# Kernel optimization log

Measured on AMD Instinct MI355X. Metric: run time of the kernel, lower is better.

## Reference

```python
import jax, jax.numpy as jnp
import numpy as np

BN_EPS = 1e-5


def setup_inputs() -> dict:
    key = jax.random.key(0)
    k1, k2, k3 = jax.random.split(key, 3)
    B, Fin, N, Fout, k = 8, 64, 4096, 128, 16
    x = jax.random.normal(k1, (B, Fin, N), dtype=jnp.float32)
    # 1x1 conv weight [Fout, 2*Fin] and bias [Fout]
    W = jax.random.normal(k2, (Fout, 2 * Fin), dtype=jnp.float32) * (1.0 / np.sqrt(2 * Fin))
    b = jax.random.normal(k3, (Fout,), dtype=jnp.float32) * 0.01
    gamma = jnp.ones((Fout,), dtype=jnp.float32)
    beta = jnp.zeros((Fout,), dtype=jnp.float32)
    return {"x": x, "W": W, "b": b, "gamma": gamma, "beta": beta, "k": k}


def reference(x, W, b, gamma, beta, k):
    # x: [B, Fin, N]
    B, Fin, N = x.shape
    xt = jnp.transpose(x, (0, 2, 1))  # [B, N, Fin]
    # pairwise squared distances [B, N, N]
    sq = jnp.sum(xt * xt, axis=-1)  # [B, N]
    dist = sq[:, :, None] + sq[:, None, :] - 2.0 * jnp.einsum("bnf,bmf->bnm", xt, xt)
    # k nearest neighbours excluding self (smallest dist is self ~ 0)
    _, idx = jax.lax.top_k(-dist, k + 1)  # [B, N, k+1]
    idx = idx[:, :, 1:]  # [B, N, k]
    # gather neighbour features: [B, N, k, Fin]
    neigh = jax.vmap(lambda pts, ids: pts[ids])(xt, idx)
    central = xt[:, :, None, :]  # [B, N, 1, Fin]
    edge = jnp.concatenate(
        [jnp.broadcast_to(central, neigh.shape), neigh - central], axis=-1
    )  # [B, N, k, 2*Fin]
    # 1x1 conv == channel contraction
    y = jnp.einsum("bnkc,oc->bnko", edge, W) + b  # [B, N, k, Fout]
    # BatchNorm2d (training-mode batch stats over B, N, k per channel)
    mean = jnp.mean(y, axis=(0, 1, 2))
    var = jnp.var(y, axis=(0, 1, 2))
    y = (y - mean) * jax.lax.rsqrt(var + BN_EPS) * gamma + beta
    y = jax.nn.relu(y)
    # max over k neighbours -> [B, Fout, N]
    out = jnp.max(y, axis=2)  # [B, N, Fout]
    return jnp.transpose(out, (0, 2, 1))
```

## Files before the change

kernel.cpp:

```cpp
#include <hip/hip_runtime.h>

#define NPTS 4096
#define FIN  64
#define FOUT 128
#define KNB  16
#define BATCH 8
#define BN_EPS 1e-5f
#define FINF 1e30f

#define OFF_SQ     (0)
#define OFF_IDX    (OFF_SQ + BATCH*NPTS*4)
#define OFF_PART   (OFF_IDX + BATCH*NPTS*KNB*4)
#define OFF_PART2  (OFF_PART + 512*FOUT*4)
#define OFF_UBAR   (OFF_PART2 + 512*FOUT*4)
#define OFF_VT     (OFF_UBAR + BATCH*NPTS*FOUT*4)

__global__ __launch_bounds__(256) void uvsq_kernel(const float* __restrict__ x, const float* __restrict__ W,
                                                   const float* __restrict__ bias,
                                                   float* __restrict__ ubar, float* __restrict__ vt,
                                                   float* __restrict__ sqout){
  const int t = threadIdx.x, l = t & 63;
  const int w = __builtin_amdgcn_readfirstlane(t >> 6);
  const int bid = blockIdx.x;
  const int b = bid & 7, grp = bid >> 3;
  const int n = grp*64 + l;
  const float* xp = x + (size_t)b*FIN*NPTS + n;
  float xc[FIN];
  float s = 0.f;
  #pragma unroll
  for (int f=0; f<FIN; ++f){ xc[f] = xp[(size_t)f*NPTS]; s = fmaf(xc[f], xc[f], s); }
  const size_t bn = (size_t)b*NPTS + n;
  if (w == 0) sqout[bn] = s;
  float* up = ubar + bn*FOUT;
  float* vp = vt   + bn*FOUT;
  for (int o = w*32; o < w*32+32; ++o){
    const float* wr = W + o*2*FIN;
    float a1=0.f, a2=0.f;
    #pragma unroll
    for (int f=0; f<FIN; ++f){ a1 = fmaf(wr[f], xc[f], a1); a2 = fmaf(wr[FIN+f], xc[f], a2); }
    up[o] = a1 - a2 + bias[o];
    vp[o] = a2;
  }
}

__global__ __launch_bounds__(256,2) void knn_kernel(const float* __restrict__ x, const float* __restrict__ sq,
                                                    int* __restrict__ idxout){
  __shared__ float xt[2*64*64];
  __shared__ float rowf[64*68];
  __shared__ float dtile[64*68];
  __shared__ float rowsq[64];
  const int t = threadIdx.x;
  const int w = t >> 6;
  const int l = t & 63;
  const int b  = blockIdx.x & 7;
  const int n0 = (blockIdx.x >> 3) * 64;
  const float* xb  = x  + (size_t)b*FIN*NPTS;
  const float* sqb = sq + b*NPTS;

  for (int j=t; j<4096; j+=256){ int row = j & 63, f = j >> 6; rowf[row*68+f] = xb[(size_t)f*NPTS + n0 + row]; }
  if (t < 64) rowsq[t] = sqb[n0 + t];

  const int c4 = (t & 15) << 2;
  const int tf = t >> 4;

  float4 pre[4];
  #pragma unroll
  for (int it=0; it<4; ++it) pre[it] = *(const float4*)(xb + (size_t)(it*16 + tf)*NPTS + c4);
  #pragma unroll
  for (int it=0; it<4; ++it){
    const int f = it*16 + tf;
    const float4 v = pre[it];
    xt[(c4+0)*64 + (f ^ c4)] = v.x;
    xt[(c4+1)*64 + (f ^ c4)] = v.y;
    xt[(c4+2)*64 + (f ^ c4)] = v.z;
    xt[(c4+3)*64 + (f ^ c4)] = v.w;
  }
  #pragma unroll
  for (int it=0; it<4; ++it) pre[it] = *(const float4*)(xb + (size_t)(it*16 + tf)*NPTS + 64 + c4);

  __syncthreads();

  const int cl = l & 15;
  const int rl = l >> 4;
  float rsq[4]; int nself[4];
  #pragma unroll
  for (int jr=0;jr<4;++jr){ int r = w*16 + rl*4 + jr; rsq[jr] = rowsq[r]; nself[jr] = n0 + r; }

  float val[16]; int idx[16];
  #pragma unroll
  for (int q=0;q<16;++q){ val[q] = FINF; idx[q] = 0; }
  const int selrow = w*16 + (l>>2);
  const int selc   = l & 3;
  const int sbase  = selrow*68 + selc;

  for (int c0=0; c0<NPTS; c0+=64){
    const int cur = (c0 >> 6) & 1;
    __syncthreads();
    {
      float* dst = xt + ((cur^1) << 12);
      #pragma unroll
      for (int it=0; it<4; ++it){
        const int f = it*16 + tf;
        const float4 v = pre[it];
        dst[(c4+0)*64 + (f ^ c4)] = v.x;
        dst[(c4+1)*64 + (f ^ c4)] = v.y;
        dst[(c4+2)*64 + (f ^ c4)] = v.z;
        dst[(c4+3)*64 + (f ^ c4)] = v.w;
      }
    }
    {
      const int cn = (c0 + 128) & (NPTS-1);
      #pragma unroll
      for (int it=0; it<4; ++it) pre[it] = *(const float4*)(xb + (size_t)(it*16 + tf)*NPTS + cn + c4);
    }
    float csq[4];
    #pragma unroll
    for (int jc=0;jc<4;++jc) csq[jc] = sqb[c0 + cl*4 + jc];

    const float* xtc = xt + (cur << 12);
    float acc[4][4];
    #pragma unroll
    for (int jc=0;jc<4;++jc){
      #pragma unroll
      for (int jr=0;jr<4;++jr) acc[jc][jr]=0.f;
    }
    #pragma unroll
    for (int i=0;i<16;++i){
      const int fp = ((i ^ cl) << 2);
      float4 xv[4], rf[4];
      #pragma unroll
      for (int jc=0;jc<4;++jc) xv[jc] = *(const float4*)&xtc[(cl*4+jc)*64 + fp];
      #pragma unroll
      for (int jr=0;jr<4;++jr) rf[jr] = *(const float4*)&rowf[(w*16+rl*4+jr)*68 + i*4];
      #pragma unroll
      for (int jc=0;jc<4;++jc){
        #pragma unroll
        for (int jr=0;jr<4;++jr){
          acc[jc][jr] = fmaf(xv[jc].x, rf[jr].x, acc[jc][jr]);
          acc[jc][jr] = fmaf(xv[jc].y, rf[jr].y, acc[jc][jr]);
          acc[jc][jr] = fmaf(xv[jc].z, rf[jr].z, acc[jc][jr]);
          acc[jc][jr] = fmaf(xv[jc].w, rf[jr].w, acc[jc][jr]);
        }
      }
    }

    #pragma unroll
    for (int jr=0;jr<4;++jr){
      float4 dd;
      dd.x = fmaf(-2.f, acc[0][jr], rsq[jr] + csq[0]);
      dd.y = fmaf(-2.f, acc[1][jr], rsq[jr] + csq[1]);
      dd.z = fmaf(-2.f, acc[2][jr], rsq[jr] + csq[2]);
      dd.w = fmaf(-2.f, acc[3][jr], rsq[jr] + csq[3]);
      if (c0 == n0){
        const int c = c0 + cl*4;
        if (c+0 == nself[jr]) dd.x = FINF;
        if (c+1 == nself[jr]) dd.y = FINF;
        if (c+2 == nself[jr]) dd.z = FINF;
        if (c+3 == nself[jr]) dd.w = FINF;
      }
      *(float4*)&dtile[(w*16 + rl*4 + jr)*68 + cl*4] = dd;
    }
    {
      const float thr = val[15];
      unsigned mask = 0;
      #pragma unroll
      for (int j=15;j>=0;--j){
        const float d = dtile[sbase + 4*j];
        mask = (mask << 1) | (d < thr ? 1u : 0u);
      }
      while (mask){
        const int j = __builtin_ctz(mask);
        mask &= mask - 1;
        const float d = dtile[sbase + 4*j];
        if (d < val[15]){
          val[15] = d; idx[15] = c0 + selc + 4*j;
          #pragma unroll
          for (int q=15;q>0;--q){
            const bool s_ = val[q] < val[q-1];
            const float tv = val[q], tu = val[q-1];
            val[q]   = s_ ? tu : tv;
            val[q-1] = s_ ? tv : tu;
            const int iv = idx[q], iu = idx[q-1];
            idx[q]   = s_ ? iu : iv;
            idx[q-1] = s_ ? iv : iu;
          }
        }
      }
    }
  }

  int myidx[4];
  #pragma unroll
  for (int round=0; round<16; ++round){
    float v = val[0]; int ii = idx[0]; int src = selc;
    #pragma unroll
    for (int mm=1; mm<4; mm<<=1){
      const float ov = __shfl_xor(v, mm);
      const int   oi = __shfl_xor(ii, mm);
      const int   os = __shfl_xor(src, mm);
      const bool take = (ov < v) || (ov == v && os < src);
      v = take ? ov : v; ii = take ? oi : ii; src = take ? os : src;
    }
    if (selc == src){
      #pragma unroll
      for (int q=0;q<15;++q){ val[q]=val[q+1]; idx[q]=idx[q+1]; }
      val[15] = FINF;
    }
    if ((round & 3) == selc) myidx[round>>2] = ii;
  }
  {
    const int bn = b*NPTS + n0 + selrow;
    int* op = idxout + (size_t)bn*KNB;
    #pragma unroll
    for (int q=0;q<4;++q) op[q*4 + selc] = myidx[q];
  }
}

__global__ __launch_bounds__(256) void gather_kernel(const float* __restrict__ vt, const float* __restrict__ ubar,
                                                     const int* __restrict__ idxnb, const float* __restrict__ gamma,
                                                     float* __restrict__ outsel, float* __restrict__ part,
                                                     float* __restrict__ part2){
  __shared__ float red[2*FOUT];
  const int t = threadIdx.x;
  const int o = t & 127;
  const int h = __builtin_amdgcn_readfirstlane(t >> 7);
  const int bid = blockIdx.x;
  const int b = bid & 7;
  const int nblk = (bid >> 3) * 64;
  const float gam = gamma[o];
  const float* vtb = vt + (size_t)b*NPTS*FOUT + o;
  float bs = 0.f, bsq = 0.f;
  for (int p=0; p<8; ++p){
    const int ng = nblk + (h*8 + p)*4;
    float selv[4];
    #pragma unroll
    for (int j=0; j<4; ++j){
      const int n  = ng + j;
      const int bn = b*NPTS + n;
      const int* ip = idxnb + (size_t)bn*KNB;
      float mx = -FINF, mn = FINF, s1 = 0.f, s2 = 0.f;
      #pragma unroll
      for (int kk=0; kk<KNB; ++kk){
        const int m = ip[kk];
        const float v = vtb[(size_t)m*FOUT];
        mx = fmaxf(mx, v); mn = fminf(mn, v); s1 += v; s2 = fmaf(v, v, s2);
      }
      const float c = ubar[(size_t)bn*FOUT + o];
      selv[j] = c + (gam >= 0.f ? mx : mn);
      bs  += fmaf(16.f, c, s1);
      bsq += fmaf(16.f*c, c, fmaf(2.f*c, s1, s2));
    }
    *(float4*)&outsel[((size_t)b*FOUT + o)*NPTS + ng] = make_float4(selv[0],selv[1],selv[2],selv[3]);
  }
  if (h == 1){ red[o] = bs; red[FOUT+o] = bsq; }
  __syncthreads();
  if (h == 0){
    part [bid*FOUT + o] = bs  + red[o];
    part2[bid*FOUT + o] = bsq + red[FOUT+o];
  }
}

__global__ __launch_bounds__(256) void applybn_kernel(float* __restrict__ out, const float* __restrict__ part,
                                                      const float* __restrict__ part2,
                                                      const float* __restrict__ gamma, const float* __restrict__ beta){
  __shared__ float red[8];
  const int bid = blockIdx.x;
  const int o = bid & 127, b = bid >> 7;
  const int t = threadIdx.x;
  float s1 = part [t*FOUT + o] + part [(t+256)*FOUT + o];
  float s2 = part2[t*FOUT + o] + part2[(t+256)*FOUT + o];
  #pragma unroll
  for (int m=1; m<64; m<<=1){ s1 += __shfl_xor(s1, m); s2 += __shfl_xor(s2, m); }
  const int w = t >> 6, l = t & 63;
  if (l == 0){ red[w] = s1; red[4+w] = s2; }
  __syncthreads();
  s1 = red[0]+red[1]+red[2]+red[3];
  s2 = red[4]+red[5]+red[6]+red[7];
  const float invM = 1.f / (float)(BATCH*NPTS*KNB);
  const float mean = s1 * invM;
  const float var  = s2 * invM - mean*mean;
  const float a = gamma[o] * rsqrtf(var + BN_EPS);
  const float c = beta[o] - mean * a;
  float4* p = (float4*)(out + ((size_t)(b*FOUT + o))*NPTS);
  #pragma unroll
  for (int q=0; q<4; ++q){
    float4 v = p[t + q*256];
    v.x = fmaxf(fmaf(a, v.x, c), 0.f);
    v.y = fmaxf(fmaf(a, v.y, c), 0.f);
    v.z = fmaxf(fmaf(a, v.z, c), 0.f);
    v.w = fmaxf(fmaf(a, v.w, c), 0.f);
    p[t + q*256] = v;
  }
}

extern "C" void kernel_launch(void* const* d_in, const int* in_sizes, int n_in,
                              void* d_out, int out_size, void* d_ws, size_t ws_size,
                              hipStream_t stream){
  const float* x     = (const float*)d_in[0];
  const float* W     = (const float*)d_in[1];
  const float* bias  = (const float*)d_in[2];
  const float* gamma = (const float*)d_in[3];
  const float* beta  = (const float*)d_in[4];
  char* ws = (char*)d_ws;
  float* sq     = (float*)(ws + OFF_SQ);
  int*   idxnb  = (int*)(ws + OFF_IDX);
  float* part   = (float*)(ws + OFF_PART);
  float* part2  = (float*)(ws + OFF_PART2);
  float* ubar   = (float*)(ws + OFF_UBAR);
  float* vt     = (float*)(ws + OFF_VT);
  float* out    = (float*)d_out;

  uvsq_kernel   <<<BATCH*NPTS/64, 256, 0, stream>>>(x, W, bias, ubar, vt, sq);
  knn_kernel    <<<BATCH*NPTS/64, 256, 0, stream>>>(x, sq, idxnb);
  gather_kernel <<<BATCH*NPTS/64, 256, 0, stream>>>(vt, ubar, idxnb, gamma, out, part, part2);
  applybn_kernel<<<BATCH*FOUT,    256, 0, stream>>>(out, part, part2, gamma, beta);
}
```

Before: 704.3 us.

## Halve kNN rows per block and single-buffer candidate tile to raise block count

The kNN kernel now handles 32 query rows per block instead of 64, which doubles the grid to 1024 blocks. Each thread computes a 4x2 tile, and the top-k selection uses 8 lanes per row with a 3-step shuffle merge. The candidate tile drops from double to single buffering in LDS, with two barriers per iteration around the refill. The aim is more blocks and lower LDS and register use for better occupancy and CU balance, at the cost of loading candidate tiles twice as often overall and losing the load/compute overlap.

```diff
diff --git a/kernel.cpp b/kernel.cpp
--- a/kernel.cpp
+++ b/kernel.cpp
@@ -45,20 +45,21 @@
 
 __global__ __launch_bounds__(256,2) void knn_kernel(const float* __restrict__ x, const float* __restrict__ sq,
                                                     int* __restrict__ idxout){
-  __shared__ float xt[2*64*64];
-  __shared__ float rowf[64*68];
-  __shared__ float dtile[64*68];
-  __shared__ float rowsq[64];
+  __shared__ float xt[64*64];
+  __shared__ float rowf[32*68];
+  __shared__ float dtile[32*68];
+  __shared__ float rowsq[32];
   const int t = threadIdx.x;
   const int w = t >> 6;
   const int l = t & 63;
   const int b  = blockIdx.x & 7;
-  const int n0 = (blockIdx.x >> 3) * 64;
+  const int n0 = (blockIdx.x >> 3) * 32;
+  const int ndiag = n0 & ~63;
   const float* xb  = x  + (size_t)b*FIN*NPTS;
   const float* sqb = sq + b*NPTS;
 
-  for (int j=t; j<4096; j+=256){ int row = j & 63, f = j >> 6; rowf[row*68+f] = xb[(size_t)f*NPTS + n0 + row]; }
-  if (t < 64) rowsq[t] = sqb[n0 + t];
+  for (int j=t; j<2048; j+=256){ int row = j & 31, f = j >> 5; rowf[row*68+f] = xb[(size_t)f*NPTS + n0 + row]; }
+  if (t < 32) rowsq[t] = sqb[n0 + t];
 
   const int c4 = (t & 15) << 2;
   const int tf = t >> 4;
@@ -82,60 +83,37 @@
 
   const int cl = l & 15;
   const int rl = l >> 4;
-  float rsq[4]; int nself[4];
-  #pragma unroll
-  for (int jr=0;jr<4;++jr){ int r = w*16 + rl*4 + jr; rsq[jr] = rowsq[r]; nself[jr] = n0 + r; }
+  const int row0 = w*8 + rl*2;
+  const float rsq0 = rowsq[row0], rsq1 = rowsq[row0+1];
+  const int nself0 = n0 + row0, nself1 = n0 + row0 + 1;
 
   float val[16]; int idx[16];
   #pragma unroll
   for (int q=0;q<16;++q){ val[q] = FINF; idx[q] = 0; }
-  const int selrow = w*16 + (l>>2);
-  const int selc   = l & 3;
+  const int selrow = w*8 + (l>>3);
+  const int selc   = l & 7;
   const int sbase  = selrow*68 + selc;
 
   for (int c0=0; c0<NPTS; c0+=64){
-    const int cur = (c0 >> 6) & 1;
-    __syncthreads();
-    {
-      float* dst = xt + ((cur^1) << 12);
-      #pragma unroll
-      for (int it=0; it<4; ++it){
-        const int f = it*16 + tf;
-        const float4 v = pre[it];
-        dst[(c4+0)*64 + (f ^ c4)] = v.x;
-        dst[(c4+1)*64 + (f ^ c4)] = v.y;
-        dst[(c4+2)*64 + (f ^ c4)] = v.z;
-        dst[(c4+3)*64 + (f ^ c4)] = v.w;
-      }
-    }
-    {
-      const int cn = (c0 + 128) & (NPTS-1);
-      #pragma unroll
-      for (int it=0; it<4; ++it) pre[it] = *(const float4*)(xb + (size_t)(it*16 + tf)*NPTS + cn + c4);
-    }
     float csq[4];
     #pragma unroll
     for (int jc=0;jc<4;++jc) csq[jc] = sqb[c0 + cl*4 + jc];
 
-    const float* xtc = xt + (cur << 12);
-    float acc[4][4];
-    #pragma unroll
-    for (int jc=0;jc<4;++jc){
-      #pragma unroll
-      for (int jr=0;jr<4;++jr) acc[jc][jr]=0.f;
-    }
+    float acc[4][2];
+    #pragma unroll
+    for (int jc=0;jc<4;++jc){ acc[jc][0]=0.f; acc[jc][1]=0.f; }
     #pragma unroll
     for (int i=0;i<16;++i){
       const int fp = ((i ^ cl) << 2);
-      float4 xv[4], rf[4];
-      #pragma unroll
-      for (int jc=0;jc<4;++jc) xv[jc] = *(const float4*)&xtc[(cl*4+jc)*64 + fp];
-      #pragma unroll
-      for (int jr=0;jr<4;++jr) rf[jr] = *(const float4*)&rowf[(w*16+rl*4+jr)*68 + i*4];
+      float4 xv[4], rf[2];
+      #pragma unroll
+      for (int jc=0;jc<4;++jc) xv[jc] = *(const float4*)&xt[(cl*4+jc)*64 + fp];
+      rf[0] = *(const float4*)&rowf[ row0   *68 + i*4];
+      rf[1] = *(const float4*)&rowf[(row0+1)*68 + i*4];
       #pragma unroll
       for (int jc=0;jc<4;++jc){
         #pragma unroll
-        for (int jr=0;jr<4;++jr){
+        for (int jr=0;jr<2;++jr){
           acc[jc][jr] = fmaf(xv[jc].x, rf[jr].x, acc[jc][jr]);
           acc[jc][jr] = fmaf(xv[jc].y, rf[jr].y, acc[jc][jr]);
           acc[jc][jr] = fmaf(xv[jc].z, rf[jr].z, acc[jc][jr]);
@@ -144,36 +122,47 @@
       }
     }
 
-    #pragma unroll
-    for (int jr=0;jr<4;++jr){
+    {
       float4 dd;
-      dd.x = fmaf(-2.f, acc[0][jr], rsq[jr] + csq[0]);
-      dd.y = fmaf(-2.f, acc[1][jr], rsq[jr] + csq[1]);
-      dd.z = fmaf(-2.f, acc[2][jr], rsq[jr] + csq[2]);
-      dd.w = fmaf(-2.f, acc[3][jr], rsq[jr] + csq[3]);
-      if (c0 == n0){
+      dd.x = fmaf(-2.f, acc[0][0], rsq0 + csq[0]);
+      dd.y = fmaf(-2.f, acc[1][0], rsq0 + csq[1]);
+      dd.z = fmaf(-2.f, acc[2][0], rsq0 + csq[2]);
+      dd.w = fmaf(-2.f, acc[3][0], rsq0 + csq[3]);
+      if (c0 == ndiag){
         const int c = c0 + cl*4;
-        if (c+0 == nself[jr]) dd.x = FINF;
-        if (c+1 == nself[jr]) dd.y = FINF;
-        if (c+2 == nself[jr]) dd.z = FINF;
-        if (c+3 == nself[jr]) dd.w = FINF;
-      }
-      *(float4*)&dtile[(w*16 + rl*4 + jr)*68 + cl*4] = dd;
+        if (c+0 == nself0) dd.x = FINF;
+        if (c+1 == nself0) dd.y = FINF;
+        if (c+2 == nself0) dd.z = FINF;
+        if (c+3 == nself0) dd.w = FINF;
+      }
+      *(float4*)&dtile[ row0   *68 + cl*4] = dd;
+      dd.x = fmaf(-2.f, acc[0][1], rsq1 + csq[0]);
+      dd.y = fmaf(-2.f, acc[1][1], rsq1 + csq[1]);
+      dd.z = fmaf(-2.f, acc[2][1], rsq1 + csq[2]);
+      dd.w = fmaf(-2.f, acc[3][1], rsq1 + csq[3]);
+      if (c0 == ndiag){
+        const int c = c0 + cl*4;
+        if (c+0 == nself1) dd.x = FINF;
+        if (c+1 == nself1) dd.y = FINF;
+        if (c+2 == nself1) dd.z = FINF;
+        if (c+3 == nself1) dd.w = FINF;
+      }
+      *(float4*)&dtile[(row0+1)*68 + cl*4] = dd;
     }
     {
       const float thr = val[15];
       unsigned mask = 0;
       #pragma unroll
-      for (int j=15;j>=0;--j){
-        const float d = dtile[sbase + 4*j];
+      for (int j=7;j>=0;--j){
+        const float d = dtile[sbase + 8*j];
         mask = (mask << 1) | (d < thr ? 1u : 0u);
       }
       while (mask){
         const int j = __builtin_ctz(mask);
         mask &= mask - 1;
-        const float d = dtile[sbase + 4*j];
+        const float d = dtile[sbase + 8*j];
         if (d < val[15]){
-          val[15] = d; idx[15] = c0 + selc + 4*j;
+          val[15] = d; idx[15] = c0 + selc + 8*j;
           #pragma unroll
           for (int q=15;q>0;--q){
             const bool s_ = val[q] < val[q-1];
@@ -187,14 +176,30 @@
         }
       }
     }
-  }
-
-  int myidx[4];
+    if (c0 + 64 < NPTS){
+      __syncthreads();
+      #pragma unroll
+      for (int it=0; it<4; ++it){
+        const int f = it*16 + tf;
+        const float4 v = pre[it];
+        xt[(c4+0)*64 + (f ^ c4)] = v.x;
+        xt[(c4+1)*64 + (f ^ c4)] = v.y;
+        xt[(c4+2)*64 + (f ^ c4)] = v.z;
+        xt[(c4+3)*64 + (f ^ c4)] = v.w;
+      }
+      const int cn = (c0 + 128) & (NPTS-1);
+      #pragma unroll
+      for (int it=0; it<4; ++it) pre[it] = *(const float4*)(xb + (size_t)(it*16 + tf)*NPTS + cn + c4);
+      __syncthreads();
+    }
+  }
+
+  int myidx[2];
   #pragma unroll
   for (int round=0; round<16; ++round){
     float v = val[0]; int ii = idx[0]; int src = selc;
     #pragma unroll
-    for (int mm=1; mm<4; mm<<=1){
+    for (int mm=1; mm<8; mm<<=1){
       const float ov = __shfl_xor(v, mm);
       const int   oi = __shfl_xor(ii, mm);
       const int   os = __shfl_xor(src, mm);
@@ -206,13 +211,13 @@
       for (int q=0;q<15;++q){ val[q]=val[q+1]; idx[q]=idx[q+1]; }
       val[15] = FINF;
     }
-    if ((round & 3) == selc) myidx[round>>2] = ii;
+    if ((round & 7) == selc) myidx[round>>3] = ii;
   }
   {
     const int bn = b*NPTS + n0 + selrow;
     int* op = idxout + (size_t)bn*KNB;
-    #pragma unroll
-    for (int q=0;q<4;++q) op[q*4 + selc] = myidx[q];
+    op[selc]     = myidx[0];
+    op[8 + selc] = myidx[1];
   }
 }
 
@@ -311,7 +316,7 @@
   float* out    = (float*)d_out;
 
   uvsq_kernel   <<<BATCH*NPTS/64, 256, 0, stream>>>(x, W, bias, ubar, vt, sq);
-  knn_kernel    <<<BATCH*NPTS/64, 256, 0, stream>>>(x, sq, idxnb);
+  knn_kernel    <<<BATCH*NPTS/32, 256, 0, stream>>>(x, sq, idxnb);
   gather_kernel <<<BATCH*NPTS/64, 256, 0, stream>>>(vt, ubar, idxnb, gamma, out, part, part2);
   applybn_kernel<<<BATCH*FOUT,    256, 0, stream>>>(out, part, part2, gamma, beta);
 }
```

Result: no change. 709.9 us (+0.8%).
